# Kernel optimization log

Hardware: AMD Instinct MI355X
Metric: run time of the kernel (lower is better)

Reference implementation:

```python
import jax, jax.numpy as jnp
import numpy as np

NL_IN = 0.5      # init kwarg nl_in
CONS = 1e-10     # epsilon added to rates
POISSON_GAIN = 20.0

def setup_inputs() -> dict:
    key = jax.random.key(0)
    k1, k2 = jax.random.split(key)
    shape = (8, 4, 28, 256, 256)  # (bs, c, s, h, w)
    spec_data = jax.random.uniform(k1, shape, dtype=jnp.float32)
    filt = jax.random.uniform(k2, shape, dtype=jnp.float32)
    return {"spec_data": spec_data, "filter": filt}

def reference(spec_data, filter):
    # cap_data = sum over (channel, spectral) dims -> [bs, h, w], then [bs, h, w, 1]
    cap = jnp.sum(spec_data * filter, axis=(1, 2))[..., None]

    # noise synthesis (need_noise=True path)
    poisson_t = jnp.full_like(cap, POISSON_GAIN * NL_IN)
    dark_t = jnp.full_like(cap, 1.0 * NL_IN)
    gauss_t = jnp.full_like(cap, 1.0 * NL_IN)
    peak = cap + CONS

    key = jax.random.key(1)
    kp, kd, kg = jax.random.split(key, 3)
    pnoisy = jax.random.poisson(kp, peak).astype(cap.dtype)
    dnoisy = jax.random.poisson(kd, dark_t).astype(cap.dtype)
    gnoisy = jax.random.normal(kg, cap.shape, dtype=cap.dtype) * gauss_t

    noisy = (pnoisy + dnoisy + gnoisy) * poisson_t / 255.0
    return (noisy, peak, dark_t, gauss_t ** 2)
```

## Files before the change

### kernel.cpp

```cpp
#include <hip/hip_runtime.h>
#include <cstdint>
#include <cstddef>

#pragma clang fp contract(off)

#define N_PIX    524288
#define CSPLANES 112
#define PLANE    65536
#define DCH      48
#define NBLK     512

struct TF2 { uint32_t a, b; };

__host__ __device__ constexpr uint32_t rotl32(uint32_t x, int d) {
  return (x << d) | (x >> (32 - d));
}

__host__ __device__ constexpr TF2 threefry(uint32_t k0, uint32_t k1,
                                           uint32_t c0, uint32_t c1) {
  uint32_t ks2 = k0 ^ k1 ^ 0x1BD11BDAu;
  uint32_t x0 = c0 + k0;
  uint32_t x1 = c1 + k1;
  const int R0[4] = {13, 15, 26, 6};
  const int R1[4] = {17, 29, 16, 24};
  for (int i = 0; i < 4; ++i) { x0 += x1; x1 = rotl32(x1, R0[i]); x1 ^= x0; }
  x0 += k1;  x1 += ks2 + 1u;
  for (int i = 0; i < 4; ++i) { x0 += x1; x1 = rotl32(x1, R1[i]); x1 ^= x0; }
  x0 += ks2; x1 += k0 + 2u;
  for (int i = 0; i < 4; ++i) { x0 += x1; x1 = rotl32(x1, R0[i]); x1 ^= x0; }
  x0 += k0;  x1 += k1 + 3u;
  for (int i = 0; i < 4; ++i) { x0 += x1; x1 = rotl32(x1, R1[i]); x1 ^= x0; }
  x0 += k1;  x1 += ks2 + 4u;
  for (int i = 0; i < 4; ++i) { x0 += x1; x1 = rotl32(x1, R0[i]); x1 ^= x0; }
  x0 += ks2; x1 += k0 + 5u;
  return TF2{x0, x1};
}

struct Chains {
  uint32_t kg0, kg1;
  uint32_t rj0a[DCH], rj0b[DCH], rj1a[DCH], rj1b[DCH];
  uint32_t kda[DCH], kdb[DCH];
  uint32_t kpa[DCH], kpb[DCH];
};

__host__ __device__ constexpr Chains make_chains() {
  Chains c{};
  TF2 kp = threefry(0u, 1u, 0u, 0u);
  TF2 kd = threefry(0u, 1u, 0u, 1u);
  TF2 kg = threefry(0u, 1u, 0u, 2u);
  c.kg0 = kg.a; c.kg1 = kg.b;
  {
    uint32_t a = kp.a, b = kp.b;
    for (int i = 0; i < DCH; ++i) {
      TF2 nk = threefry(a, b, 0u, 0u);
      TF2 s0 = threefry(a, b, 0u, 1u);
      TF2 s1 = threefry(a, b, 0u, 2u);
      c.rj0a[i] = s0.a; c.rj0b[i] = s0.b;
      c.rj1a[i] = s1.a; c.rj1b[i] = s1.b;
      a = nk.a; b = nk.b;
    }
  }
  {
    uint32_t a = kd.a, b = kd.b;
    for (int i = 0; i < DCH; ++i) {
      TF2 nk = threefry(a, b, 0u, 0u);
      TF2 sk = threefry(a, b, 0u, 1u);
      c.kda[i] = sk.a; c.kdb[i] = sk.b;
      a = nk.a; b = nk.b;
    }
  }
  {
    uint32_t a = kp.a, b = kp.b;
    for (int i = 0; i < DCH; ++i) {
      TF2 nk = threefry(a, b, 0u, 0u);
      TF2 sk = threefry(a, b, 0u, 1u);
      c.kpa[i] = sk.a; c.kpb[i] = sk.b;
      a = nk.a; b = nk.b;
    }
  }
  return c;
}

__constant__ Chains G = make_chains();

__device__ inline float u01(uint32_t k0, uint32_t k1, uint32_t j) {
  TF2 r = threefry(k0, k1, 0u, j);
  uint32_t bits = r.a ^ r.b;
  return __uint_as_float((bits >> 9) | 0x3F800000u) - 1.0f;
}

__device__ inline float xla_lgamma(float x_in) {
  float z = x_in - 1.0f;
  float x = 1.0f;
  x = x + 676.520368121885098567009190444019f    / ((z + 0.0f) + 1.0f);
  x = x + (-1259.13921672240287047156078755283f) / ((z + 1.0f) + 1.0f);
  x = x + 771.3234287776530788486528258894f      / ((z + 2.0f) + 1.0f);
  x = x + (-176.61502916214059906584551354f)     / ((z + 3.0f) + 1.0f);
  x = x + 12.507343278686904814458936853f        / ((z + 4.0f) + 1.0f);
  x = x + (-0.13857109526572011689554707f)       / ((z + 5.0f) + 1.0f);
  x = x + 9.984369578019570859563e-6f            / ((z + 6.0f) + 1.0f);
  x = x + 1.50563273514931155834e-7f             / ((z + 7.0f) + 1.0f);
  float t = 7.5f + z;
  float log_t = 2.0149030205422647f + log1pf(z / 7.5f);
  return 0.91893853320467274178f + ((z + 0.5f) - t / log_t) * log_t + logf(x);
}

__device__ inline float xla_erfinv(float xx) {
  float w = -log1pf(-(xx * xx));
  float p;
  if (w < 5.0f) {
    float ww = w - 2.5f;
    p = 2.81022636e-08f;
    p = 3.43273939e-07f + p * ww;
    p = -3.5233877e-06f + p * ww;
    p = -4.39150654e-06f + p * ww;
    p = 0.00021858087f + p * ww;
    p = -0.00125372503f + p * ww;
    p = -0.00417768164f + p * ww;
    p = 0.246640727f + p * ww;
    p = 1.50140941f + p * ww;
  } else {
    float ww = sqrtf(w) - 3.0f;
    p = -0.000200214257f;
    p = 0.000100950558f + p * ww;
    p = 0.00134934322f + p * ww;
    p = -0.00367342844f + p * ww;
    p = 0.00573950773f + p * ww;
    p = -0.0076224613f + p * ww;
    p = 0.00943887047f + p * ww;
    p = 1.00167406f + p * ww;
    p = 2.83297682f + p * ww;
  }
  return p * xx;
}

__device__ inline float xla_normal(uint32_t j) {
  const float lo = -0.999999940395355224609375f;
  float f = u01(G.kg0, G.kg1, j);
  float u = f * (1.0f - lo) + lo;
  u = fmaxf(lo, u);
  return 1.41421356237309504880f * xla_erfinv(u);
}

__device__ inline int knuth_sample(const uint32_t* ka, const uint32_t* kb,
                                   uint32_t j, float lam) {
  const float neg = -lam;
  int k = 0;
  float lp = 0.0f;
  #pragma unroll 1
  for (int i = 0; i < DCH; ++i) {
    if (!(lp > neg)) break;
    ++k;
    float uu = u01(ka[i], kb[i], j);
    lp = lp + logf(uu);
  }
  return k - 1;
}

struct RejC { float lam, loglam, a, b, inva, vr; };

__device__ inline RejC make_rc(float lam) {
  RejC rc;
  rc.lam = lam;
  rc.loglam = logf(lam);
  rc.b = 0.931f + 2.53f * sqrtf(lam);
  rc.a = -0.059f + 0.02483f * rc.b;
  rc.inva = 1.1239f + 1.1328f / (rc.b - 3.4f);
  rc.vr = 0.9277f - 3.6224f / (rc.b - 2.0f);
  return rc;
}

__device__ inline bool rej_step(const RejC& rc, uint32_t j, int i, float* kout) {
  float u = u01(G.rj0a[i], G.rj0b[i], j) - 0.5f;
  float v = u01(G.rj1a[i], G.rj1b[i], j);
  float us = 0.5f - fabsf(u);
  float k = floorf(((2.0f * rc.a / us + rc.b) * u + rc.lam) + 0.43f);
  *kout = k;
  bool accept1 = (us >= 0.07f) && (v <= rc.vr);
  if (accept1) return true;
  bool reject = (k < 0.0f) || ((us < 0.013f) && (v > us));
  if (reject) return false;
  float s = logf(v * rc.inva / (rc.a / (us * us) + rc.b));
  float t = (-rc.lam + k * rc.loglam) - xla_lgamma(k + 1.0f);
  return s <= t;
}

__device__ inline unsigned first_accept(const RejC& rc, uint32_t j) {
  unsigned F = DCH;
  #pragma unroll 1
  for (int i = 0; i < DCH; ++i) {
    float kc;
    if (rej_step(rc, j, i, &kc)) { F = (unsigned)(i + 1); break; }
  }
  return F;
}

__device__ inline float resolve_pix(const RejC& rc, float peak, uint32_t j, int T) {
  if (peak >= 10.0f) {
    float kk = -1.0f;
    #pragma unroll 1
    for (int i = T - 1; i >= 0; --i) {
      float kc;
      if (rej_step(rc, j, i, &kc)) { kk = kc; break; }
    }
    return (float)(int)kk;
  } else if (peak <= 0.0f) {
    return 0.0f;
  } else {
    return (float)knuth_sample(G.kpa, G.kpb, j, peak);
  }
}

__global__ __launch_bounds__(1024, 8) void fused_kernel(const float* __restrict__ spec,
                                                        const float* __restrict__ filt,
                                                        float* __restrict__ out,
                                                        unsigned* __restrict__ sync) {
  const int tid = threadIdx.x;
  const int pixbase = blockIdx.x << 10;
  const int b_img = pixbase >> 16;
  const int hw = (pixbase & 65535) + tid;
  const size_t base = (size_t)b_img * ((size_t)CSPLANES * PLANE) + (size_t)hw;
  const float* sp = spec + base;
  const float* fp = filt + base;

  float a = 0.f;
  #pragma unroll 1
  for (int c = 0; c < CSPLANES; c += 16) {
    float ss[16], ff[16];
    #pragma unroll
    for (int i = 0; i < 16; ++i) ss[i] = sp[(size_t)(c + i) * PLANE];
    #pragma unroll
    for (int i = 0; i < 16; ++i) ff[i] = fp[(size_t)(c + i) * PLANE];
    #pragma unroll
    for (int i = 0; i < 16; ++i) a = a + ss[i] * ff[i];
  }

  const uint32_t j = (uint32_t)(pixbase + tid);
  const float pk = a + 1e-10f;
  const float d = (float)knuth_sample(G.kda, G.kdb, j, 0.5f);
  const float g = xla_normal(j) * 0.5f;
  const RejC rc = make_rc(pk);
  unsigned F = first_accept(rc, j);

  for (int off = 32; off; off >>= 1) {
    unsigned o = (unsigned)__shfl_down((int)F, off, 64);
    F = F > o ? F : o;
  }
  __shared__ unsigned sred[16];
  __shared__ int sT;
  if ((tid & 63) == 0) sred[tid >> 6] = F;
  __syncthreads();
  if (tid == 0) {
    unsigned m = sred[0];
    #pragma unroll
    for (int i = 1; i < 16; ++i) m = m > sred[i] ? m : sred[i];
    __hip_atomic_fetch_max(&sync[0], m, __ATOMIC_RELAXED, __HIP_MEMORY_SCOPE_AGENT);
    __hip_atomic_fetch_add(&sync[1], 1u, __ATOMIC_ACQ_REL, __HIP_MEMORY_SCOPE_AGENT);
    while (__hip_atomic_load(&sync[1], __ATOMIC_ACQUIRE, __HIP_MEMORY_SCOPE_AGENT) < (unsigned)NBLK) {
      __builtin_amdgcn_s_sleep(8);
    }
    sT = (int)__hip_atomic_load(&sync[0], __ATOMIC_RELAXED, __HIP_MEMORY_SCOPE_AGENT);
  }
  __syncthreads();
  const int T = sT;

  const float pv = resolve_pix(rc, pk, j, T);
  const float n = ((pv + d) + g) * 10.0f / 255.0f;

  out[j]             = n;
  out[N_PIX + j]     = pk;
  out[2 * N_PIX + j] = 0.5f;
  out[3 * N_PIX + j] = 0.25f;
}

extern "C" void kernel_launch(void* const* d_in, const int* in_sizes, int n_in,
                              void* d_out, int out_size, void* d_ws, size_t ws_size,
                              hipStream_t stream) {
  (void)in_sizes; (void)n_in; (void)out_size; (void)ws_size;
  const float* spec = (const float*)d_in[0];
  const float* filt = (const float*)d_in[1];
  float* out = (float*)d_out;
  unsigned* sync = (unsigned*)d_ws;
  (void)hipMemsetAsync(d_ws, 0, 2 * sizeof(unsigned), stream);
  hipLaunchKernelGGL(fused_kernel, dim3(NBLK), dim3(1024), 0, stream,
                     spec, filt, out, sync);
}
```

Baseline: 542.6 us.

## Split fused kernel into reduce, max, and resolve kernels with float4 loads

```diff
diff --git a/kernel.cpp b/kernel.cpp
--- a/kernel.cpp
+++ b/kernel.cpp
@@ -8,7 +8,6 @@
 #define CSPLANES 112
 #define PLANE    65536
 #define DCH      48
-#define NBLK     512
 
 struct TF2 { uint32_t a, b; };
 
@@ -211,64 +210,77 @@
   }
 }
 
-__global__ __launch_bounds__(1024, 8) void fused_kernel(const float* __restrict__ spec,
-                                                        const float* __restrict__ filt,
-                                                        float* __restrict__ out,
-                                                        unsigned* __restrict__ sync) {
+__global__ __launch_bounds__(256) void reduce_kernel(const float* __restrict__ spec,
+                                                     const float* __restrict__ filt,
+                                                     float* __restrict__ out) {
   const int tid = threadIdx.x;
   const int pixbase = blockIdx.x << 10;
   const int b_img = pixbase >> 16;
-  const int hw = (pixbase & 65535) + tid;
+  const int hw = (pixbase & 65535) + (tid << 2);
   const size_t base = (size_t)b_img * ((size_t)CSPLANES * PLANE) + (size_t)hw;
   const float* sp = spec + base;
   const float* fp = filt + base;
 
-  float a = 0.f;
+  float4 acc = make_float4(0.f, 0.f, 0.f, 0.f);
   #pragma unroll 1
-  for (int c = 0; c < CSPLANES; c += 16) {
-    float ss[16], ff[16];
+  for (int c = 0; c < CSPLANES; c += 8) {
+    float4 ss[8], ff[8];
     #pragma unroll
-    for (int i = 0; i < 16; ++i) ss[i] = sp[(size_t)(c + i) * PLANE];
+    for (int i = 0; i < 8; ++i) ss[i] = *reinterpret_cast<const float4*>(sp + (size_t)(c + i) * PLANE);
     #pragma unroll
-    for (int i = 0; i < 16; ++i) ff[i] = fp[(size_t)(c + i) * PLANE];
+    for (int i = 0; i < 8; ++i) ff[i] = *reinterpret_cast<const float4*>(fp + (size_t)(c + i) * PLANE);
+    __builtin_amdgcn_sched_group_barrier(0x020, 16, 0);
     #pragma unroll
-    for (int i = 0; i < 16; ++i) a = a + ss[i] * ff[i];
-  }
-
-  const uint32_t j = (uint32_t)(pixbase + tid);
-  const float pk = a + 1e-10f;
-  const float d = (float)knuth_sample(G.kda, G.kdb, j, 0.5f);
-  const float g = xla_normal(j) * 0.5f;
+    for (int i = 0; i < 8; ++i) {
+      acc.x = acc.x + ss[i].x * ff[i].x;
+      acc.y = acc.y + ss[i].y * ff[i].y;
+      acc.z = acc.z + ss[i].z * ff[i].z;
+      acc.w = acc.w + ss[i].w * ff[i].w;
+    }
+    __builtin_amdgcn_sched_group_barrier(0x002, 64, 0);
+  }
+
+  const int j = pixbase + (tid << 2);
+  float4 pk = make_float4(acc.x + 1e-10f, acc.y + 1e-10f,
+                          acc.z + 1e-10f, acc.w + 1e-10f);
+  *reinterpret_cast<float4*>(out + N_PIX + j) = pk;
+}
+
+__global__ __launch_bounds__(256) void fmax_kernel(const float* __restrict__ out,
+                                                   unsigned* __restrict__ sync) {
+  const int j = (blockIdx.x << 8) + threadIdx.x;
+  const float pk = out[N_PIX + j];
   const RejC rc = make_rc(pk);
-  unsigned F = first_accept(rc, j);
+  unsigned F = first_accept(rc, (uint32_t)j);
 
   for (int off = 32; off; off >>= 1) {
     unsigned o = (unsigned)__shfl_down((int)F, off, 64);
     F = F > o ? F : o;
   }
-  __shared__ unsigned sred[16];
-  __shared__ int sT;
-  if ((tid & 63) == 0) sred[tid >> 6] = F;
+  __shared__ unsigned sred[4];
+  if ((threadIdx.x & 63) == 0) sred[threadIdx.x >> 6] = F;
   __syncthreads();
-  if (tid == 0) {
+  if (threadIdx.x == 0) {
     unsigned m = sred[0];
     #pragma unroll
-    for (int i = 1; i < 16; ++i) m = m > sred[i] ? m : sred[i];
+    for (int i = 1; i < 4; ++i) m = m > sred[i] ? m : sred[i];
     __hip_atomic_fetch_max(&sync[0], m, __ATOMIC_RELAXED, __HIP_MEMORY_SCOPE_AGENT);
-    __hip_atomic_fetch_add(&sync[1], 1u, __ATOMIC_ACQ_REL, __HIP_MEMORY_SCOPE_AGENT);
-    while (__hip_atomic_load(&sync[1], __ATOMIC_ACQUIRE, __HIP_MEMORY_SCOPE_AGENT) < (unsigned)NBLK) {
-      __builtin_amdgcn_s_sleep(8);
-    }
-    sT = (int)__hip_atomic_load(&sync[0], __ATOMIC_RELAXED, __HIP_MEMORY_SCOPE_AGENT);
-  }
-  __syncthreads();
-  const int T = sT;
-
-  const float pv = resolve_pix(rc, pk, j, T);
+  }
+}
+
+__global__ __launch_bounds__(256) void resolve_kernel(float* __restrict__ out,
+                                                      const unsigned* __restrict__ sync) {
+  const int j = (blockIdx.x << 8) + threadIdx.x;
+  const int T = (int)__hip_atomic_load(&sync[0], __ATOMIC_RELAXED, __HIP_MEMORY_SCOPE_AGENT);
+  const float pk = out[N_PIX + j];
+
+  const float d = (float)knuth_sample(G.kda, G.kdb, (uint32_t)j, 0.5f);
+  const float g = xla_normal((uint32_t)j) * 0.5f;
+  const RejC rc = make_rc(pk);
+  const float pv = resolve_pix(rc, pk, (uint32_t)j, T);
   const float n = ((pv + d) + g) * 10.0f / 255.0f;
 
   out[j]             = n;
-  out[N_PIX + j]     = pk;
   out[2 * N_PIX + j] = 0.5f;
   out[3 * N_PIX + j] = 0.25f;
 }
@@ -282,6 +294,7 @@
   float* out = (float*)d_out;
   unsigned* sync = (unsigned*)d_ws;
   (void)hipMemsetAsync(d_ws, 0, 2 * sizeof(unsigned), stream);
-  hipLaunchKernelGGL(fused_kernel, dim3(NBLK), dim3(1024), 0, stream,
-                     spec, filt, out, sync);
-}
+  hipLaunchKernelGGL(reduce_kernel, dim3(512), dim3(256), 0, stream, spec, filt, out);
+  hipLaunchKernelGGL(fmax_kernel, dim3(2048), dim3(256), 0, stream, out, sync);
+  hipLaunchKernelGGL(resolve_kernel, dim3(2048), dim3(256), 0, stream, out, sync);
+}
```

New measurement: 502.6 us. -7.4%, faster.
